# Kernel optimization log

Measured on AMD Instinct MI355X. Metric: run time of the kernel, lower is better.

Reference implementation:

```python
import jax, jax.numpy as jnp
import numpy as np

N = 20000          # num nodes
E = 320000         # num edges
D = 128            # in_channels (= out_channels)
H = 8              # num_heads
HD = D // H        # head_dim = 16


def setup_inputs() -> dict:
    key = jax.random.key(0)
    ks = jax.random.split(key, 10)
    s = 0.05
    return {
        "x": jax.random.normal(ks[0], (N, D), jnp.float32),
        "edges": jax.random.randint(ks[1], (E, 2), 0, N, jnp.int64),
        "Wp": jax.random.normal(ks[2], (D, D), jnp.float32) * s,
        "bp": jax.random.normal(ks[3], (D,), jnp.float32) * s,
        "Wm": jax.random.normal(ks[4], (D, D), jnp.float32) * s,
        "bm": jax.random.normal(ks[5], (D,), jnp.float32) * s,
        "W1": jax.random.normal(ks[6], (D, 2 * D), jnp.float32) * s,
        "b1": jax.random.normal(ks[7], (D,), jnp.float32) * s,
        "W2": jax.random.normal(ks[8], (D, D), jnp.float32) * s,
        "b2": jax.random.normal(ks[9], (D,), jnp.float32) * s,
    }


def reference(x, edges, Wp, bp, Wm, bm, W1, b1, W2, b2):
    # edges: [E,2] -> row (src), col (dst)
    row, col = edges[:, 0], edges[:, 1]
    src = x[row]                       # [E, D] gather
    dst = x[col]                       # [E, D] gather
    # shared preprocess Linear for q, k, v (key == value == dst features)
    q = src @ Wp.T + bp                # [E, D]
    kv = dst @ Wp.T + bp               # [E, D]
    # view(E, -1, H, HD).transpose(1,2) with seq_len 1 -> effectively [E, H, HD]
    q = q.reshape(E, H, HD)
    k = kv.reshape(E, H, HD)
    v = k
    # original attention() misreads axes: contracts over HEAD axis, scale 1/sqrt(H),
    # softmax over the head_dim axis -> scores [E, HD, HD]
    scores = jnp.einsum("ehn,ehm->enm", q, k) / jnp.sqrt(jnp.float32(H))
    prob = jax.nn.softmax(scores, axis=-1)          # [E, HD, HD]
    out = jnp.einsum("enm,ehm->ehn", prob, v)       # [E, H, HD]
    # view(E, HD*H, 1) then 1x1 Conv1d merge == Linear
    msg = out.reshape(E, H * HD) @ Wm.T + bm        # [E, D]
    # scatter-sum aggregate by destination node (empty -> 0, matches torch loop)
    agg = jax.ops.segment_sum(msg, col, num_segments=N)  # [N, D]
    h = jnp.concatenate([x, agg], axis=1)           # [N, 2D]
    h = jax.nn.relu(h @ W1.T + b1)
    return h @ W2.T + b2                            # [N, D]
```

## Files before the change

### kernel.cpp

```cpp
#include <hip/hip_runtime.h>

#define NN 20000
#define EE 320000
#define DEGCAP 64

typedef _Float16 half4_t __attribute__((ext_vector_type(4)));
typedef float f32x4 __attribute__((ext_vector_type(4)));

#define MFMA16F16 __builtin_amdgcn_mfma_f32_16x16x16f16

__global__ __launch_bounds__(256) void setup_kernel(
    int4* __restrict__ countv,
    const float* __restrict__ Wp, const float* __restrict__ Wm,
    const float* __restrict__ W1, const float* __restrict__ W2,
    _Float16* __restrict__ wpt, _Float16* __restrict__ wmt,
    _Float16* __restrict__ w1t, _Float16* __restrict__ w2t) {
  const int b = blockIdx.x, t = threadIdx.x;
  if (b < 20) {
    countv[b * 256 + t] = int4{0, 0, 0, 0};
    return;
  }
  const int tid = (b - 20) * 256 + t;
  const float* W; _Float16* dst; int K, l;
  if (tid < 16384)      { W = Wp; dst = wpt; K = 128; l = tid; }
  else if (tid < 32768) { W = Wm; dst = wmt; K = 128; l = tid - 16384; }
  else if (tid < 65536) { W = W1; dst = w1t; K = 256; l = tid - 32768; }
  else                  { W = W2; dst = w2t; K = 128; l = tid - 65536; }
  const int j = l & 3, n = (l >> 2) & 15, g = (l >> 6) & 3;
  const int ot = (l >> 8) & 7, kt = l >> 11;
  const int k = kt * 16 + 4 * g + j, o = ot * 16 + n;
  dst[l] = (_Float16)W[o * K + k];
}

__global__ __launch_bounds__(256) void bin_proj_kernel(
    const int* __restrict__ edges, int* __restrict__ count,
    int* __restrict__ srow,
    const float* __restrict__ x, const _Float16* __restrict__ wpt,
    const float* __restrict__ bp, _Float16* __restrict__ ph) {
  const int b = blockIdx.x, t = threadIdx.x;
  if (b < 1250) {
    const int e = b * 256 + t;
    const int row = edges[2 * e];
    const int col = edges[2 * e + 1];
    const int slot = atomicAdd(&count[col], 1);
    if (slot < DEGCAP) srow[col * DEGCAP + slot] = row;
    return;
  }
  const int wv = __builtin_amdgcn_readfirstlane(t >> 6), lane = t & 63;
  const int n = lane & 15, g = lane >> 4;
  const int rb = (b - 1250) * 16;
  const int arow = rb + n;

  half4_t a[8];
#pragma unroll
  for (int kt = 0; kt < 8; ++kt) {
    const float4 xv = *(const float4*)&x[(size_t)arow * 128 + kt * 16 + 4 * g];
    half4_t h; h[0] = (_Float16)xv.x; h[1] = (_Float16)xv.y;
    h[2] = (_Float16)xv.z; h[3] = (_Float16)xv.w;
    a[kt] = h;
  }
  const f32x4 zero = {0.f, 0.f, 0.f, 0.f};
#pragma unroll
  for (int oi = 0; oi < 2; ++oi) {
    const int ot = wv * 2 + oi;
    f32x4 acc = zero;
#pragma unroll
    for (int kt = 0; kt < 8; ++kt) {
      const half4_t bb = *(const half4_t*)&wpt[(((kt * 8 + ot) * 4 + g) << 6) + n * 4];
      acc = MFMA16F16(a[kt], bb, acc, 0, 0, 0);
    }
    const float bpv = bp[ot * 16 + n];
#pragma unroll
    for (int r = 0; r < 4; ++r) {
      const int nrow = rb + 4 * g + r;
      ph[(size_t)nrow * 128 + n * 8 + ot] = (_Float16)(acc[r] + bpv);
    }
  }
}

__global__ __launch_bounds__(512) void edge_node_kernel(
    const _Float16* __restrict__ ph, const int* __restrict__ count,
    const int* __restrict__ srow,
    const float* __restrict__ x,
    const _Float16* __restrict__ wmt, const float* __restrict__ bm,
    const _Float16* __restrict__ w1t, const float* __restrict__ b1,
    const _Float16* __restrict__ w2t, const float* __restrict__ b2,
    float* __restrict__ out) {
  __shared__ _Float16 agl[16 * 132];
  __shared__ _Float16 mh[16 * 132];
  __shared__ _Float16 hh[16 * 132];
  const int t = threadIdx.x;
  const int wv = __builtin_amdgcn_readfirstlane(t >> 6);
  const int lane = t & 63;
  const int n = lane & 15, g = lane >> 4;
  const int rb = blockIdx.x * 16;
  const f32x4 zero = {0.f, 0.f, 0.f, 0.f};
  const float c2 = 0.5101268320290106f;
  const int laneoff = n * 8 + 4 * g;

#define GATHER(DST)                                                          \
  {                                                                          \
    const int ii_ = (pre < deg) ? pre : (deg - 1);                           \
    DST = *(const half4_t*)&ph[((unsigned)srow[base + ii_] << 7) + laneoff]; \
    ++pre;                                                                   \
  }
#define PROC(Q)                                                              \
  {                                                                          \
    f32x4 s_ = MFMA16F16(ka, Q, zero, 0, 0, 0);                              \
    const float p0_ = __builtin_amdgcn_exp2f((float)s_[0] * c2);             \
    const float p1_ = __builtin_amdgcn_exp2f((float)s_[1] * c2);             \
    const float p2_ = __builtin_amdgcn_exp2f((float)s_[2] * c2);             \
    const float p3_ = __builtin_amdgcn_exp2f((float)s_[3] * c2);             \
    float sum_ = (p0_ + p1_) + (p2_ + p3_);                                  \
    sum_ += __shfl_xor(sum_, 16, 64);                                        \
    sum_ += __shfl_xor(sum_, 32, 64);                                        \
    const float inv_ = __builtin_amdgcn_rcpf(sum_);                          \
    psum[0] = fmaf(p0_, inv_, psum[0]);                                      \
    psum[1] = fmaf(p1_, inv_, psum[1]);                                      \
    psum[2] = fmaf(p2_, inv_, psum[2]);                                      \
    psum[3] = fmaf(p3_, inv_, psum[3]);                                      \
  }

  for (int ci = 0; ci < 2; ++ci) {
    const int col = rb + wv * 2 + ci;
    const _Float16* __restrict__ pc = ph + ((unsigned)col << 7);
    half4_t ka{};
    if (g < 2) ka = *(const half4_t*)&pc[n * 8 + 4 * g];
    half4_t a2{};
    if (n < 8) {
#pragma unroll
      for (int j = 0; j < 4; ++j) a2[j] = pc[(4 * g + j) * 8 + n];
    }
    const int deg0 = count[col];
    const int deg = (deg0 < DEGCAP) ? deg0 : DEGCAP;
    const int base = col * DEGCAP;
    f32x4 psum = zero;
    if (deg > 0) {
      int pre = 0;
      half4_t q0, q1, q2, q3;
      GATHER(q0) GATHER(q1) GATHER(q2) GATHER(q3)
      int i = 0;
      for (; i + 4 <= deg; i += 4) {
        PROC(q0) GATHER(q0)
        PROC(q1) GATHER(q1)
        PROC(q2) GATHER(q2)
        PROC(q3) GATHER(q3)
      }
      const int rem = deg - i;
      if (rem > 0) PROC(q0)
      if (rem > 1) PROC(q1)
      if (rem > 2) PROC(q2)
    }
    half4_t pb;
#pragma unroll
    for (int r = 0; r < 4; ++r) pb[r] = (_Float16)psum[r];
    f32x4 o = MFMA16F16(a2, pb, zero, 0, 0, 0);
    if (g < 2) {
#pragma unroll
      for (int r = 0; r < 4; ++r)
        agl[(wv * 2 + ci) * 132 + (4 * g + r) * 16 + n] = (_Float16)o[r];
    }
  }
#undef GATHER
#undef PROC

  float cnt_r[4];
#pragma unroll
  for (int r = 0; r < 4; ++r)
    cnt_r[r] = (float)count[rb + 4 * g + r];

  __syncthreads();

  const int ot = wv;
  half4_t am[8];
#pragma unroll
  for (int kt = 0; kt < 8; ++kt)
    am[kt] = *(const half4_t*)&agl[n * 132 + kt * 16 + 4 * g];
  {
    f32x4 acc = zero;
#pragma unroll
    for (int kt = 0; kt < 8; ++kt) {
      const half4_t b = *(const half4_t*)&wmt[(((kt * 8 + ot) * 4 + g) << 6) + n * 4];
      acc = MFMA16F16(am[kt], b, acc, 0, 0, 0);
    }
    const float bmv = bm[ot * 16 + n];
#pragma unroll
    for (int r = 0; r < 4; ++r)
      mh[(4 * g + r) * 132 + ot * 16 + n] = (_Float16)(acc[r] + cnt_r[r] * bmv);
  }

  half4_t ah[16];
#pragma unroll
  for (int kt = 0; kt < 8; ++kt) {
    const float4 xv = *(const float4*)&x[(size_t)(rb + n) * 128 + kt * 16 + 4 * g];
    half4_t h; h[0] = (_Float16)xv.x; h[1] = (_Float16)xv.y;
    h[2] = (_Float16)xv.z; h[3] = (_Float16)xv.w;
    ah[kt] = h;
  }
  __syncthreads();
#pragma unroll
  for (int kt = 0; kt < 8; ++kt)
    ah[8 + kt] = *(const half4_t*)&mh[n * 132 + kt * 16 + 4 * g];
  {
    f32x4 acc = zero;
#pragma unroll
    for (int kt = 0; kt < 16; ++kt) {
      const half4_t b = *(const half4_t*)&w1t[(((kt * 8 + ot) * 4 + g) << 6) + n * 4];
      acc = MFMA16F16(ah[kt], b, acc, 0, 0, 0);
    }
    const float b1v = b1[ot * 16 + n];
#pragma unroll
    for (int r = 0; r < 4; ++r)
      hh[(4 * g + r) * 132 + ot * 16 + n] = (_Float16)fmaxf(acc[r] + b1v, 0.f);
  }

  __syncthreads();
  half4_t ay[8];
#pragma unroll
  for (int kt = 0; kt < 8; ++kt)
    ay[kt] = *(const half4_t*)&hh[n * 132 + kt * 16 + 4 * g];
  {
    f32x4 acc = zero;
#pragma unroll
    for (int kt = 0; kt < 8; ++kt) {
      const half4_t b = *(const half4_t*)&w2t[(((kt * 8 + ot) * 4 + g) << 6) + n * 4];
      acc = MFMA16F16(ay[kt], b, acc, 0, 0, 0);
    }
    const float b2v = b2[ot * 16 + n];
#pragma unroll
    for (int r = 0; r < 4; ++r)
      out[(size_t)(rb + 4 * g + r) * 128 + ot * 16 + n] = acc[r] + b2v;
  }
}

extern "C" void kernel_launch(void* const* d_in, const int* in_sizes, int n_in,
                              void* d_out, int out_size, void* d_ws, size_t ws_size,
                              hipStream_t stream) {
  const float* x = (const float*)d_in[0];
  const int* edges = (const int*)d_in[1];
  const float* Wp = (const float*)d_in[2];
  const float* bp = (const float*)d_in[3];
  const float* Wm = (const float*)d_in[4];
  const float* bm = (const float*)d_in[5];
  const float* W1 = (const float*)d_in[6];
  const float* b1 = (const float*)d_in[7];
  const float* W2 = (const float*)d_in[8];
  const float* b2 = (const float*)d_in[9];
  float* out = (float*)d_out;

  _Float16* ph   = (_Float16*)d_ws;
  _Float16* wpt  = ph + (size_t)NN * 128;
  _Float16* wmt  = wpt + 16384;
  _Float16* w1t  = wmt + 16384;
  _Float16* w2t  = w1t + 32768;
  int* count = (int*)(w2t + 16384);
  int* srow  = count + 20480;

  setup_kernel<<<340, 256, 0, stream>>>((int4*)count, Wp, Wm, W1, W2,
                                        wpt, wmt, w1t, w2t);
  bin_proj_kernel<<<2500, 256, 0, stream>>>(edges, count, srow,
                                            x, wpt, bp, ph);
  edge_node_kernel<<<NN / 16, 512, 0, stream>>>(ph, count, srow, x,
                                                wmt, bm, w1t, b1, w2t, b2, out);
}
```

Measured before the change: 82.65 us.

## Give each wave one destination node and broadcast neighbor indices via readlane

The fused edge/node kernel now handles 8 destination nodes per block (one per wave) instead of 16 (two per wave in sequence), doubling the grid. Each wave preloads its node's 64 neighbor indices with one coalesced load and picks each index with readlane, replacing a dependent global index load per gather. The node MLP stages still use 16-row MFMA tiles but only 8 rows are real, so half the MFMA work is wasted and the weights are reloaded per block twice as often.

```diff
diff --git a/kernel.cpp b/kernel.cpp
--- a/kernel.cpp
+++ b/kernel.cpp
@@ -86,22 +86,38 @@
     const _Float16* __restrict__ w1t, const float* __restrict__ b1,
     const _Float16* __restrict__ w2t, const float* __restrict__ b2,
     float* __restrict__ out) {
-  __shared__ _Float16 agl[16 * 132];
-  __shared__ _Float16 mh[16 * 132];
-  __shared__ _Float16 hh[16 * 132];
+  __shared__ _Float16 agl[8 * 132];
+  __shared__ _Float16 mh[8 * 132];
+  __shared__ _Float16 hh[8 * 132];
   const int t = threadIdx.x;
   const int wv = __builtin_amdgcn_readfirstlane(t >> 6);
   const int lane = t & 63;
   const int n = lane & 15, g = lane >> 4;
-  const int rb = blockIdx.x * 16;
+  const int rb = blockIdx.x * 8;
   const f32x4 zero = {0.f, 0.f, 0.f, 0.f};
   const float c2 = 0.5101268320290106f;
   const int laneoff = n * 8 + 4 * g;
 
+  const int col = rb + wv;
+  const _Float16* __restrict__ pc = ph + ((unsigned)col << 7);
+  half4_t ka{};
+  if (g < 2) ka = *(const half4_t*)&pc[n * 8 + 4 * g];
+  half4_t a2{};
+  if (n < 8) {
+#pragma unroll
+    for (int j = 0; j < 4; ++j) a2[j] = pc[(4 * g + j) * 8 + n];
+  }
+  const int deg0 = count[col];
+  const int deg = (deg0 < DEGCAP) ? deg0 : DEGCAP;
+  const int degm1 = deg - 1;
+  const int slots = srow[col * DEGCAP + lane];
+  f32x4 psum = zero;
+
 #define GATHER(DST)                                                          \
   {                                                                          \
-    const int ii_ = (pre < deg) ? pre : (deg - 1);                           \
-    DST = *(const half4_t*)&ph[((unsigned)srow[base + ii_] << 7) + laneoff]; \
+    const int ii_ = (pre < deg) ? pre : degm1;                               \
+    const int row_ = __builtin_amdgcn_readlane(slots, ii_);                  \
+    DST = *(const half4_t*)&ph[((unsigned)row_ << 7) + laneoff];             \
     ++pre;                                                                   \
   }
 #define PROC(Q)                                                              \
@@ -121,36 +137,26 @@
     psum[3] = fmaf(p3_, inv_, psum[3]);                                      \
   }
 
-  for (int ci = 0; ci < 2; ++ci) {
-    const int col = rb + wv * 2 + ci;
-    const _Float16* __restrict__ pc = ph + ((unsigned)col << 7);
-    half4_t ka{};
-    if (g < 2) ka = *(const half4_t*)&pc[n * 8 + 4 * g];
-    half4_t a2{};
-    if (n < 8) {
-#pragma unroll
-      for (int j = 0; j < 4; ++j) a2[j] = pc[(4 * g + j) * 8 + n];
-    }
-    const int deg0 = count[col];
-    const int deg = (deg0 < DEGCAP) ? deg0 : DEGCAP;
-    const int base = col * DEGCAP;
-    f32x4 psum = zero;
-    if (deg > 0) {
-      int pre = 0;
-      half4_t q0, q1, q2, q3;
-      GATHER(q0) GATHER(q1) GATHER(q2) GATHER(q3)
-      int i = 0;
-      for (; i + 4 <= deg; i += 4) {
-        PROC(q0) GATHER(q0)
-        PROC(q1) GATHER(q1)
-        PROC(q2) GATHER(q2)
-        PROC(q3) GATHER(q3)
-      }
-      const int rem = deg - i;
-      if (rem > 0) PROC(q0)
-      if (rem > 1) PROC(q1)
-      if (rem > 2) PROC(q2)
-    }
+  if (deg > 0) {
+    int pre = 0;
+    half4_t q0, q1, q2, q3;
+    GATHER(q0) GATHER(q1) GATHER(q2) GATHER(q3)
+    int i = 0;
+    for (; i + 4 <= deg; i += 4) {
+      PROC(q0) GATHER(q0)
+      PROC(q1) GATHER(q1)
+      PROC(q2) GATHER(q2)
+      PROC(q3) GATHER(q3)
+    }
+    const int rem = deg - i;
+    if (rem > 0) PROC(q0)
+    if (rem > 1) PROC(q1)
+    if (rem > 2) PROC(q2)
+  }
+#undef GATHER
+#undef PROC
+
+  {
     half4_t pb;
 #pragma unroll
     for (int r = 0; r < 4; ++r) pb[r] = (_Float16)psum[r];
@@ -158,24 +164,23 @@
     if (g < 2) {
 #pragma unroll
       for (int r = 0; r < 4; ++r)
-        agl[(wv * 2 + ci) * 132 + (4 * g + r) * 16 + n] = (_Float16)o[r];
-    }
-  }
-#undef GATHER
-#undef PROC
+        agl[wv * 132 + (4 * g + r) * 16 + n] = (_Float16)o[r];
+    }
+  }
 
   float cnt_r[4];
 #pragma unroll
   for (int r = 0; r < 4; ++r)
-    cnt_r[r] = (float)count[rb + 4 * g + r];
+    cnt_r[r] = (float)count[rb + ((4 * g + r) & 7)];
 
   __syncthreads();
 
   const int ot = wv;
+  const int nl = n & 7;
   half4_t am[8];
 #pragma unroll
   for (int kt = 0; kt < 8; ++kt)
-    am[kt] = *(const half4_t*)&agl[n * 132 + kt * 16 + 4 * g];
+    am[kt] = *(const half4_t*)&agl[nl * 132 + kt * 16 + 4 * g];
   {
     f32x4 acc = zero;
 #pragma unroll
@@ -184,15 +189,17 @@
       acc = MFMA16F16(am[kt], b, acc, 0, 0, 0);
     }
     const float bmv = bm[ot * 16 + n];
-#pragma unroll
-    for (int r = 0; r < 4; ++r)
-      mh[(4 * g + r) * 132 + ot * 16 + n] = (_Float16)(acc[r] + cnt_r[r] * bmv);
+    if (g < 2) {
+#pragma unroll
+      for (int r = 0; r < 4; ++r)
+        mh[(4 * g + r) * 132 + ot * 16 + n] = (_Float16)(acc[r] + cnt_r[r] * bmv);
+    }
   }
 
   half4_t ah[16];
 #pragma unroll
   for (int kt = 0; kt < 8; ++kt) {
-    const float4 xv = *(const float4*)&x[(size_t)(rb + n) * 128 + kt * 16 + 4 * g];
+    const float4 xv = *(const float4*)&x[(size_t)(rb + nl) * 128 + kt * 16 + 4 * g];
     half4_t h; h[0] = (_Float16)xv.x; h[1] = (_Float16)xv.y;
     h[2] = (_Float16)xv.z; h[3] = (_Float16)xv.w;
     ah[kt] = h;
@@ -200,7 +207,7 @@
   __syncthreads();
 #pragma unroll
   for (int kt = 0; kt < 8; ++kt)
-    ah[8 + kt] = *(const half4_t*)&mh[n * 132 + kt * 16 + 4 * g];
+    ah[8 + kt] = *(const half4_t*)&mh[nl * 132 + kt * 16 + 4 * g];
   {
     f32x4 acc = zero;
 #pragma unroll
@@ -209,16 +216,18 @@
       acc = MFMA16F16(ah[kt], b, acc, 0, 0, 0);
     }
     const float b1v = b1[ot * 16 + n];
-#pragma unroll
-    for (int r = 0; r < 4; ++r)
-      hh[(4 * g + r) * 132 + ot * 16 + n] = (_Float16)fmaxf(acc[r] + b1v, 0.f);
+    if (g < 2) {
+#pragma unroll
+      for (int r = 0; r < 4; ++r)
+        hh[(4 * g + r) * 132 + ot * 16 + n] = (_Float16)fmaxf(acc[r] + b1v, 0.f);
+    }
   }
 
   __syncthreads();
   half4_t ay[8];
 #pragma unroll
   for (int kt = 0; kt < 8; ++kt)
-    ay[kt] = *(const half4_t*)&hh[n * 132 + kt * 16 + 4 * g];
+    ay[kt] = *(const half4_t*)&hh[nl * 132 + kt * 16 + 4 * g];
   {
     f32x4 acc = zero;
 #pragma unroll
@@ -227,9 +236,11 @@
       acc = MFMA16F16(ay[kt], b, acc, 0, 0, 0);
     }
     const float b2v = b2[ot * 16 + n];
-#pragma unroll
-    for (int r = 0; r < 4; ++r)
-      out[(size_t)(rb + 4 * g + r) * 128 + ot * 16 + n] = acc[r] + b2v;
+    if (g < 2) {
+#pragma unroll
+      for (int r = 0; r < 4; ++r)
+        out[(size_t)(rb + 4 * g + r) * 128 + ot * 16 + n] = acc[r] + b2v;
+    }
   }
 }
 
@@ -260,6 +271,6 @@
                                         wpt, wmt, w1t, w2t);
   bin_proj_kernel<<<2500, 256, 0, stream>>>(edges, count, srow,
                                             x, wpt, bp, ph);
-  edge_node_kernel<<<NN / 16, 512, 0, stream>>>(ph, count, srow, x,
-                                                wmt, bm, w1t, b1, w2t, b2, out);
-}
+  edge_node_kernel<<<NN / 8, 512, 0, stream>>>(ph, count, srow, x,
+                                               wmt, bm, w1t, b1, w2t, b2, out);
+}
```

Result: slower. 99.20 us (+20.0%).

## Interleave two destination nodes per wave and fetch edge slots via readlane

Applied to the files above, without the earlier changes.

Each wave now processes its two destination nodes at once, interleaving gathers and softmax MFMA work across both columns so more independent loads are in flight. Source indices are loaded once per column as a wave-wide vector and broadcast with readlane, which replaces a dependent scalar global load per edge. Iterations past a node's degree are masked by zeroing the reciprocal. The cost is wasted work when the two degrees differ, plus extra registers for the second column's state.

```diff
diff --git a/kernel.cpp b/kernel.cpp
--- a/kernel.cpp
+++ b/kernel.cpp
@@ -98,15 +98,42 @@
   const float c2 = 0.5101268320290106f;
   const int laneoff = n * 8 + 4 * g;
 
-#define GATHER(DST)                                                          \
+  const int col0 = rb + wv * 2, col1 = col0 + 1;
+  const _Float16* __restrict__ pc0 = ph + ((unsigned)col0 << 7);
+  const _Float16* __restrict__ pc1 = ph + ((unsigned)col1 << 7);
+  half4_t ka0{}, ka1{};
+  if (g < 2) {
+    ka0 = *(const half4_t*)&pc0[n * 8 + 4 * g];
+    ka1 = *(const half4_t*)&pc1[n * 8 + 4 * g];
+  }
+  half4_t a20{}, a21{};
+  if (n < 8) {
+#pragma unroll
+    for (int j = 0; j < 4; ++j) {
+      a20[j] = pc0[(4 * g + j) * 8 + n];
+      a21[j] = pc1[(4 * g + j) * 8 + n];
+    }
+  }
+  const int d0raw = count[col0], d1raw = count[col1];
+  const int deg0 = (d0raw < DEGCAP) ? d0raw : DEGCAP;
+  const int deg1 = (d1raw < DEGCAP) ? d1raw : DEGCAP;
+  const int dm0 = (deg0 > 0) ? deg0 - 1 : 0;
+  const int dm1 = (deg1 > 0) ? deg1 - 1 : 0;
+  const int maxdeg = (deg0 > deg1) ? deg0 : deg1;
+  const int slots0 = srow[col0 * DEGCAP + lane];
+  const int slots1 = srow[col1 * DEGCAP + lane];
+  f32x4 psum0 = zero, psum1 = zero;
+
+#define GATHER(DST, SLOTS, DM, IDX)                                          \
   {                                                                          \
-    const int ii_ = (pre < deg) ? pre : (deg - 1);                           \
-    DST = *(const half4_t*)&ph[((unsigned)srow[base + ii_] << 7) + laneoff]; \
-    ++pre;                                                                   \
-  }
-#define PROC(Q)                                                              \
+    const int ii_ = ((IDX) < (DM)) ? (IDX) : (DM);                           \
+    int row_ = __builtin_amdgcn_readlane(SLOTS, ii_);                        \
+    row_ = ((unsigned)row_ < NN) ? row_ : 0;        \
+    DST = *(const half4_t*)&ph[((unsigned)row_ << 7) + laneoff];             \
+  }
+#define PROC(Q, KA, PSUM, IDX, DEG)                                          \
   {                                                                          \
-    f32x4 s_ = MFMA16F16(ka, Q, zero, 0, 0, 0);                              \
+    f32x4 s_ = MFMA16F16(KA, Q, zero, 0, 0, 0);                              \
     const float p0_ = __builtin_amdgcn_exp2f((float)s_[0] * c2);             \
     const float p1_ = __builtin_amdgcn_exp2f((float)s_[1] * c2);             \
     const float p2_ = __builtin_amdgcn_exp2f((float)s_[2] * c2);             \
@@ -114,55 +141,50 @@
     float sum_ = (p0_ + p1_) + (p2_ + p3_);                                  \
     sum_ += __shfl_xor(sum_, 16, 64);                                        \
     sum_ += __shfl_xor(sum_, 32, 64);                                        \
-    const float inv_ = __builtin_amdgcn_rcpf(sum_);                          \
-    psum[0] = fmaf(p0_, inv_, psum[0]);                                      \
-    psum[1] = fmaf(p1_, inv_, psum[1]);                                      \
-    psum[2] = fmaf(p2_, inv_, psum[2]);                                      \
-    psum[3] = fmaf(p3_, inv_, psum[3]);                                      \
-  }
-
-  for (int ci = 0; ci < 2; ++ci) {
-    const int col = rb + wv * 2 + ci;
-    const _Float16* __restrict__ pc = ph + ((unsigned)col << 7);
-    half4_t ka{};
-    if (g < 2) ka = *(const half4_t*)&pc[n * 8 + 4 * g];
-    half4_t a2{};
-    if (n < 8) {
-#pragma unroll
-      for (int j = 0; j < 4; ++j) a2[j] = pc[(4 * g + j) * 8 + n];
-    }
-    const int deg0 = count[col];
-    const int deg = (deg0 < DEGCAP) ? deg0 : DEGCAP;
-    const int base = col * DEGCAP;
-    f32x4 psum = zero;
-    if (deg > 0) {
-      int pre = 0;
-      half4_t q0, q1, q2, q3;
-      GATHER(q0) GATHER(q1) GATHER(q2) GATHER(q3)
-      int i = 0;
-      for (; i + 4 <= deg; i += 4) {
-        PROC(q0) GATHER(q0)
-        PROC(q1) GATHER(q1)
-        PROC(q2) GATHER(q2)
-        PROC(q3) GATHER(q3)
-      }
-      const int rem = deg - i;
-      if (rem > 0) PROC(q0)
-      if (rem > 1) PROC(q1)
-      if (rem > 2) PROC(q2)
-    }
-    half4_t pb;
-#pragma unroll
-    for (int r = 0; r < 4; ++r) pb[r] = (_Float16)psum[r];
-    f32x4 o = MFMA16F16(a2, pb, zero, 0, 0, 0);
-    if (g < 2) {
-#pragma unroll
-      for (int r = 0; r < 4; ++r)
-        agl[(wv * 2 + ci) * 132 + (4 * g + r) * 16 + n] = (_Float16)o[r];
+    const float inv_ =                                                       \
+        ((IDX) < (DEG)) ? __builtin_amdgcn_rcpf(sum_) : 0.f;                 \
+    PSUM[0] = fmaf(p0_, inv_, PSUM[0]);                                      \
+    PSUM[1] = fmaf(p1_, inv_, PSUM[1]);                                      \
+    PSUM[2] = fmaf(p2_, inv_, PSUM[2]);                                      \
+    PSUM[3] = fmaf(p3_, inv_, PSUM[3]);                                      \
+  }
+
+  if (maxdeg > 0) {
+    half4_t qA0, qA1, qB0, qB1;
+    GATHER(qA0, slots0, dm0, 0) GATHER(qB0, slots1, dm1, 0)
+    GATHER(qA1, slots0, dm0, 1) GATHER(qB1, slots1, dm1, 1)
+    int i = 0;
+    for (; i + 2 <= maxdeg; i += 2) {
+      PROC(qA0, ka0, psum0, i, deg0)     GATHER(qA0, slots0, dm0, i + 2)
+      PROC(qB0, ka1, psum1, i, deg1)     GATHER(qB0, slots1, dm1, i + 2)
+      PROC(qA1, ka0, psum0, i + 1, deg0) GATHER(qA1, slots0, dm0, i + 3)
+      PROC(qB1, ka1, psum1, i + 1, deg1) GATHER(qB1, slots1, dm1, i + 3)
+    }
+    if (i < maxdeg) {
+      PROC(qA0, ka0, psum0, i, deg0)
+      PROC(qB0, ka1, psum1, i, deg1)
     }
   }
 #undef GATHER
 #undef PROC
+
+  {
+    half4_t pb0, pb1;
+#pragma unroll
+    for (int r = 0; r < 4; ++r) {
+      pb0[r] = (_Float16)psum0[r];
+      pb1[r] = (_Float16)psum1[r];
+    }
+    f32x4 o0 = MFMA16F16(a20, pb0, zero, 0, 0, 0);
+    f32x4 o1 = MFMA16F16(a21, pb1, zero, 0, 0, 0);
+    if (g < 2) {
+#pragma unroll
+      for (int r = 0; r < 4; ++r) {
+        agl[(wv * 2) * 132 + (4 * g + r) * 16 + n] = (_Float16)o0[r];
+        agl[(wv * 2 + 1) * 132 + (4 * g + r) * 16 + n] = (_Float16)o1[r];
+      }
+    }
+  }
 
   float cnt_r[4];
 #pragma unroll
```

Measured after the change: 78.74 us. 4.7% less time.
